# Kernel optimization log

Hardware: AMD Instinct MI355X
Metric: run time of the kernel (lower is better)

## Reference

```python
import jax, jax.numpy as jnp
import numpy as np

ALPHA = 4.0  # spikingjelly surrogate.Sigmoid default

@jax.custom_vjp
def spike(x):
    return (x >= 0.0).astype(x.dtype)

def _spike_fwd(x):
    return spike(x), x

def _spike_bwd(x, g):
    s = jax.nn.sigmoid(ALPHA * x)
    return (g * ALPHA * s * (1.0 - s),)

spike.defvjp(_spike_fwd, _spike_bwd)

def lif(x, v0, v_th=1.0, tau=2.0):
    # Multi-step LIF over leading time axis. v' = v + (x - v)/tau; hard reset to 0; detach_reset.
    def step(v, xt):
        v = v + (xt - v) / tau
        s = spike(v - v_th)
        v = v * (1.0 - jax.lax.stop_gradient(s))
        return v, s
    v_end, s = jax.lax.scan(step, v0, x)
    return s, v_end

def bn_eval(x, gamma, beta, mean, var, eps=1e-5):
    # x: [T,B,C,N], stats over channel dim C (axis 2)
    inv = gamma / jnp.sqrt(var + eps)
    return x * inv.reshape(1, 1, -1, 1) + (beta - mean * inv).reshape(1, 1, -1, 1)

def setup_inputs() -> dict:
    key = jax.random.key(0)
    ks = jax.random.split(key, 24)
    T, B, C, H, W = 4, 16, 512, 16, 16
    d = {}
    d['x'] = jax.random.normal(ks[0], (T, B, C, H, W), dtype=jnp.float32)
    d['res_attn'] = jnp.zeros((1,), dtype=jnp.float32)
    sc = 1.0 / np.sqrt(C)
    for i, p in enumerate(['q', 'k', 'v']):
        d[p + '_w'] = jax.random.normal(ks[1 + i], (C, C), dtype=jnp.float32) * sc
    names = ['q', 'k', 'v', 'p']
    for i, p in enumerate(names):
        d[p + '_gamma'] = jax.random.uniform(ks[4 + i], (C,), minval=0.8, maxval=1.2, dtype=jnp.float32)
        d[p + '_beta'] = jax.random.normal(ks[8 + i], (C,), dtype=jnp.float32) * 0.1
        d[p + '_mean'] = jax.random.normal(ks[12 + i], (C,), dtype=jnp.float32) * 0.1
        d[p + '_var'] = jax.random.uniform(ks[16 + i], (C,), minval=0.5, maxval=1.5, dtype=jnp.float32)
    d['p_w'] = jax.random.normal(ks[20], (C, C), dtype=jnp.float32) * sc
    d['p_b'] = jax.random.normal(ks[21], (C,), dtype=jnp.float32) * 0.02
    return d

def reference(x, res_attn, q_w, q_gamma, q_beta, q_mean, q_var,
              k_w, k_gamma, k_beta, k_mean, k_var,
              v_w, v_gamma, v_beta, v_mean, v_var,
              p_w, p_b, p_gamma, p_beta, p_mean, p_var):
    T, B, C, H, W = x.shape
    N = H * W
    xf = x.reshape(T, B, C, N)
    v0 = jnp.zeros((B, C, N), dtype=x.dtype)

    def qkv_branch(w, g, b, m, va):
        y = jnp.einsum('oc,tbcn->tbon', w, xf)  # 1x1 conv over flattened T*B
        y = bn_eval(y, g, b, m, va)
        s, _ = lif(y, v0)
        return s

    q = qkv_branch(q_w, q_gamma, q_beta, q_mean, q_var)
    k = qkv_branch(k_w, k_gamma, k_beta, k_mean, k_var)
    v = qkv_branch(v_w, v_gamma, v_beta, v_mean, v_var)

    kv = jnp.einsum('tbcn,tbcm->tbnm', k, v)           # k^T @ v : [T,B,N,N]
    a = jnp.einsum('tbcn,tbnm->tbcm', q, kv) * 0.125   # q @ (k^T v), scale
    a, _ = lif(a, v0, v_th=0.5)                        # attn_lif

    y = jnp.einsum('oc,tbcn->tbon', p_w, a) + p_b.reshape(1, 1, -1, 1)
    y = bn_eval(y, p_gamma, p_beta, p_mean, p_var).reshape(T, B, C, H, W)

    v0_sp = jnp.zeros((B, C, H, W), dtype=x.dtype)
    s1, v_end = lif(y, v0_sp)      # first proj_lif call
    s2, _ = lif(s1, v_end)         # second proj_lif call: membrane state persists (stateful node)
    return s2, v
```

## Files before the change

kernel.cpp:

```cpp
#include <hip/hip_runtime.h>
#include <hip/hip_bf16.h>

#define TT 4
#define BB 16
#define CC 512
#define NN 256

typedef short short8 __attribute__((ext_vector_type(8)));
typedef _Float16 h8 __attribute__((ext_vector_type(8)));
typedef float f32x4 __attribute__((ext_vector_type(4)));
typedef float fl4 __attribute__((ext_vector_type(4)));
typedef unsigned short us4 __attribute__((ext_vector_type(4)));

__device__ __forceinline__ unsigned short bf_hi(float x) {
    unsigned u = __float_as_uint(x);
    return (unsigned short)((u + 0x7FFFu + ((u >> 16) & 1u)) >> 16);
}
__device__ __forceinline__ float bf_f(unsigned short h) {
    return __uint_as_float(((unsigned)h) << 16);
}
__device__ __forceinline__ void glds16(const void* g, void* l) {
    __builtin_amdgcn_global_load_lds(
        (const __attribute__((address_space(1))) unsigned int*)g,
        (__attribute__((address_space(3))) unsigned int*)l, 16, 0, 0);
}
__device__ __forceinline__ int csw(int c, int rkey) {
    return (c & ~63) | ((((c >> 3) & 7) ^ (rkey & 7)) << 3) | (c & 7);
}

__global__ __launch_bounds__(256) void prep_k(
    const float* __restrict__ x,
    const float* __restrict__ w0, const float* __restrict__ w1,
    const float* __restrict__ w2, const float* __restrict__ w3,
    unsigned short* __restrict__ xh, unsigned short* __restrict__ xl,
    unsigned short* __restrict__ wsplit)
{
    const int bid = blockIdx.x;
    const int tid = threadIdx.x;
    if (bid < 4096) {
        __shared__ float Tt[64][33];
        const int tb = bid >> 6, rem = bid & 63;
        const int c0 = (rem >> 3) * 64, n0 = (rem & 7) * 32;
        const int t = tb >> 4, b = tb & 15;
        {
            int row = tid >> 2, seg = tid & 3;
            const float* sp = x + ((size_t)tb * CC + c0 + row) * NN + n0 + seg * 8;
            fl4 v0 = *(const fl4*)sp;
            fl4 v1 = *(const fl4*)(sp + 4);
#pragma unroll
            for (int j = 0; j < 4; ++j) {
                Tt[row][seg * 8 + j] = v0[j];
                Tt[row][seg * 8 + 4 + j] = v1[j];
            }
        }
        __syncthreads();
        {
            int n = tid >> 3, co = tid & 7;
            int c = c0 + co * 8;
            short8 hi, lo;
#pragma unroll
            for (int j = 0; j < 8; ++j) {
                float f = Tt[co * 8 + j][n];
                unsigned short h = bf_hi(f);
                hi[j] = (short)h;
                lo[j] = (short)bf_hi(f - bf_f(h));
            }
            int nn = n0 + n;
            int key = (nn & 1) * 4 + t;
            size_t dst = (((size_t)b * NN + nn) * TT + t) * CC
                       + (c & ~63) + (((((c >> 3) & 7) ^ (key & 7))) << 3);
            *(short8*)(xh + dst) = hi;
            *(short8*)(xl + dst) = lo;
        }
    } else {
        const int wb = bid - 4096;
        const int m = wb >> 7;
        const int idx = wb & 127;
        const float* src = (m == 0) ? w0 : (m == 1) ? w1 : (m == 2) ? w2 : w3;
        unsigned short* dh = wsplit + (size_t)m * 2 * CC * CC;
        unsigned short* dl = dh + (size_t)CC * CC;
        const int flat = idx * 2048 + tid * 8;
        const int o = flat >> 9, c = flat & 511;
        const float* sp = src + flat;
        fl4 v0 = *(const fl4*)sp;
        fl4 v1 = *(const fl4*)(sp + 4);
        short8 hi, lo;
#pragma unroll
        for (int j = 0; j < 8; ++j) {
            float f = (j < 4) ? v0[j] : v1[j - 4];
            unsigned short h = bf_hi(f);
            hi[j] = (short)h;
            lo[j] = (short)bf_hi(f - bf_f(h));
        }
        size_t dst = (size_t)o * CC + (c & ~63) + ((((c >> 3) & 7) ^ (o & 7)) << 3);
        *(short8*)(dh + dst) = hi;
        *(short8*)(dl + dst) = lo;
    }
}

__global__ __launch_bounds__(256, 4) void gemm_qkv_f(
    const unsigned short* __restrict__ w8,
    const unsigned short* __restrict__ Bh, const unsigned short* __restrict__ Bl,
    const float* __restrict__ qg, const float* __restrict__ qb,
    const float* __restrict__ qm, const float* __restrict__ qva,
    const float* __restrict__ kg, const float* __restrict__ kbe,
    const float* __restrict__ km, const float* __restrict__ kva,
    const float* __restrict__ vg, const float* __restrict__ vb,
    const float* __restrict__ vm, const float* __restrict__ vva,
    const float* __restrict__ qw, const float* __restrict__ kw,
    const float* __restrict__ vw, const float* __restrict__ xf,
    unsigned short* __restrict__ qo, unsigned short* __restrict__ ktr,
    unsigned short* __restrict__ vtr, float* __restrict__ outv)
{
    const int bid = blockIdx.x;
    const int orig = (bid & 7) * 384 + (bid >> 3);
    const int cb = orig / 12;
    const int ob = orig - cb * 12;
    const int mat = ob >> 2;
    const int o0 = (ob & 3) * 128;
    const int col0 = cb * 64;
    const int b  = cb >> 4;
    const int n0 = (cb & 15) * 16;
    const unsigned short* Ah = w8 + (size_t)mat * 2 * CC * CC;
    const unsigned short* Alg = Ah + (size_t)CC * CC;

    const int tid = threadIdx.x, lane = tid & 63, wid = tid >> 6;
    const int l16 = lane & 15, kb = lane >> 4;
    const int sx = l16 & 7;

    __shared__ __align__(16) char raw[32768];

    const int srow = lane >> 3, sslot = lane & 7;
    const unsigned short* sect =
        (wid == 0) ? Ah + (size_t)o0 * CC :
        (wid == 1) ? Ah + (size_t)(o0 + 64) * CC :
        (wid == 2) ? Bh + (size_t)col0 * CC :
                     Bl + (size_t)col0 * CC;
    const unsigned short* gsrc = sect + (size_t)srow * CC + sslot * 8;
    char* ldsb = raw + wid * 8192;

    f32x4 acc[2][4];
#pragma unroll
    for (int r = 0; r < 2; ++r)
#pragma unroll
        for (int c = 0; c < 4; ++c) acc[r][c] = (f32x4){0.f, 0.f, 0.f, 0.f};

    for (int ks = 0; ks < 8; ++ks) {
        const int k0 = ks * 64;
        short8 alv[2][2];
#pragma unroll
        for (int ksub = 0; ksub < 2; ++ksub)
#pragma unroll
            for (int r = 0; r < 2; ++r)
                alv[ksub][r] = *(const short8*)(Alg
                    + (size_t)(o0 + wid * 32 + r * 16 + l16) * CC
                    + k0 + (((ksub * 4 + kb) ^ sx) << 3));
#pragma unroll
        for (int i = 0; i < 8; ++i)
            glds16(gsrc + (size_t)(i * 8) * CC + k0, ldsb + i * 1024);
        __syncthreads();
#pragma unroll
        for (int ksub = 0; ksub < 2; ++ksub) {
            const int soff = ((ksub * 4 + kb) ^ sx) << 4;
            short8 ah[2], bh[4], bl[4];
#pragma unroll
            for (int r = 0; r < 2; ++r) {
                const int ra = (wid * 32 + r * 16 + l16) * 128 + soff;
                ah[r] = *(const short8*)(raw + ra);
            }
#pragma unroll
            for (int c = 0; c < 4; ++c) {
                const int rb = (c * 16 + l16) * 128 + soff;
                bh[c] = *(const short8*)(raw + 16384 + rb);
                bl[c] = *(const short8*)(raw + 24576 + rb);
            }
#pragma unroll
            for (int r = 0; r < 2; ++r)
#pragma unroll
                for (int c = 0; c < 4; ++c)
                    acc[r][c] = __builtin_amdgcn_mfma_f32_16x16x32_bf16(ah[r], bh[c], acc[r][c], 0, 0, 0);
#pragma unroll
            for (int r = 0; r < 2; ++r)
#pragma unroll
                for (int c = 0; c < 4; ++c)
                    acc[r][c] = __builtin_amdgcn_mfma_f32_16x16x32_bf16(alv[ksub][r], bh[c], acc[r][c], 0, 0, 0);
#pragma unroll
            for (int r = 0; r < 2; ++r)
#pragma unroll
                for (int c = 0; c < 4; ++c)
                    acc[r][c] = __builtin_amdgcn_mfma_f32_16x16x32_bf16(ah[r], bl[c], acc[r][c], 0, 0, 0);
        }
        __syncthreads();
    }

    float* Yf = (float*)raw;
#pragma unroll
    for (int r = 0; r < 2; ++r)
#pragma unroll
        for (int c = 0; c < 4; ++c) {
            const int col = c * 16 + l16;
#pragma unroll
            for (int g = 0; g < 4; ++g) {
                const int row = wid * 32 + r * 16 + kb * 4 + g;
                Yf[row * 64 + (col ^ (((row >> 2) & 7) << 2))] = acc[r][c][g];
            }
        }
    __syncthreads();

    const float* gg = (mat == 0) ? qg : (mat == 1) ? kg : vg;
    const float* be = (mat == 0) ? qb : (mat == 1) ? kbe : vb;
    const float* mu = (mat == 0) ? qm : (mat == 1) ? km : vm;
    const float* va = (mat == 0) ? qva : (mat == 1) ? kva : vva;
    const float* wsel = (mat == 0) ? qw : (mat == 1) ? kw : vw;

    const int lo2  = tid >> 3;
    const int rsel = (tid >> 2) & 1;
    const int ln2  = tid & 3;
    const float M1 = 2e-4f;

    float inv[2], bbv[2];
#pragma unroll
    for (int i = 0; i < 2; ++i) {
        int oo = o0 + lo2 * 4 + rsel * 2 + i;
        double invd = (double)gg[oo] / sqrt((double)va[oo] + 1e-5);
        inv[i] = (float)invd;
        bbv[i] = (float)((double)be[oo] - (double)mu[oo] * invd);
    }

    unsigned long long s1b = 0;
    unsigned fmask = 0;
#pragma unroll
    for (int i = 0; i < 2; ++i) {
        const int row = lo2 * 4 + rsel * 2 + i;
        const int rk = ((row >> 2) & 7) << 2;
#pragma unroll
        for (int j = 0; j < 4; ++j) {
            fl4 yv = *(const fl4*)&Yf[row * 64 + (((ln2 * 4 + j) * 4) ^ rk)];
            float vv = 0.f;
#pragma unroll
            for (int t = 0; t < TT; ++t) {
                float yy = yv[t] * inv[i] + bbv[i];
                vv += (yy - vv) * 0.5f;
                float d = vv - 1.0f;
                if (d < M1 && d > -M1) fmask |= 1u << (i * 4 + j);
                if (d >= 0.0f) { s1b |= 1ull << ((i * 4 + j) * 4 + t); vv = 0.f; }
            }
        }
    }

    unsigned long long ball = __ballot(fmask != 0);
    while (ball) {
        int src = __ffsll(ball) - 1;
        ball &= ball - 1;
        unsigned fm = (unsigned)__shfl((int)fmask, src);
        int slo2 = wid * 8 + (src >> 3);
        int srsel = (src >> 2) & 1, sln = src & 3;
        while (fm) {
            int cell = __ffs(fm) - 1;
            fm &= fm - 1;
            int ci = cell >> 2, cj = cell & 3;
            int oo = o0 + slo2 * 4 + srsel * 2 + ci, nn = n0 + sln * 4 + cj;
            double a0 = 0, a1 = 0, a2 = 0, a3 = 0;
            const float* wrow = wsel + (size_t)oo * CC;
            for (int c = lane; c < CC; c += 64) {
                double wv = (double)wrow[c];
                a0 += wv * (double)xf[(((size_t)(0 * BB + b) * CC + c) * NN) + nn];
                a1 += wv * (double)xf[(((size_t)(1 * BB + b) * CC + c) * NN) + nn];
                a2 += wv * (double)xf[(((size_t)(2 * BB + b) * CC + c) * NN) + nn];
                a3 += wv * (double)xf[(((size_t)(3 * BB + b) * CC + c) * NN) + nn];
            }
#pragma unroll
            for (int off = 32; off > 0; off >>= 1) {
                a0 += __shfl_xor(a0, off);
                a1 += __shfl_xor(a1, off);
                a2 += __shfl_xor(a2, off);
                a3 += __shfl_xor(a3, off);
            }
            if (lane == src) {
                double inv_ = (double)gg[oo] / sqrt((double)va[oo] + 1e-5);
                double bb_  = (double)be[oo] - (double)mu[oo] * inv_;
                s1b &= ~(0xFull << (cell * 4));
                double aa[4] = {a0, a1, a2, a3};
                double vv = 0.0;
#pragma unroll
                for (int t = 0; t < TT; ++t) {
                    double yy = aa[t] * inv_ + bb_;
                    vv += (yy - vv) * 0.5;
                    if (vv >= 1.0) { s1b |= 1ull << (cell * 4 + t); vv = 0.0; }
                }
            }
        }
    }

    if (mat == 0) {
#pragma unroll
        for (int t = 0; t < TT; ++t) {
            const size_t tb = (size_t)(t * BB + b);
#pragma unroll
            for (int i = 0; i < 2; ++i) {
                us4 pk;
#pragma unroll
                for (int j = 0; j < 4; ++j)
                    pk[j] = ((s1b >> ((i * 4 + j) * 4 + t)) & 1ull) ? (unsigned short)0x3C00 : (unsigned short)0;
                *(us4*)(qo + (tb * CC + o0 + lo2 * 4 + rsel * 2 + i) * NN + n0 + ln2 * 4) = pk;
            }
        }
    } else {
        unsigned short* tr = (mat == 1) ? ktr : vtr;
        unsigned short* Tss = (unsigned short*)raw;
        __syncthreads();
#pragma unroll
        for (int t = 0; t < TT; ++t)
#pragma unroll
            for (int j = 0; j < 4; ++j) {
                unsigned p0 = ((s1b >> ((0 * 4 + j) * 4 + t)) & 1ull) ? 0x3F80u : 0u;
                unsigned p1 = ((s1b >> ((1 * 4 + j) * 4 + t)) & 1ull) ? 0x3F80u : 0u;
                *(unsigned*)&Tss[t * 2176 + (ln2 * 4 + j) * 136 + lo2 * 4 + rsel * 2] =
                    p0 | (p1 << 16);
            }
        __syncthreads();
        {
            const int nrow = tid >> 4, seg = tid & 15;
#pragma unroll
            for (int t = 0; t < TT; ++t) {
                const unsigned short* sp = Tss + t * 2176 + nrow * 136 + seg * 8;
                short8 w0 = *(const short8*)sp;
                unsigned short* dst = tr + ((size_t)(t * BB + b) * NN + n0 + nrow) * CC + o0 + seg * 8;
                *(short8*)dst = w0;
            }
        }
        if (mat == 2) {
#pragma unroll
            for (int t = 0; t < TT; ++t) {
                const size_t tb = (size_t)(t * BB + b);
#pragma unroll
                for (int i = 0; i < 2; ++i) {
                    fl4 f;
#pragma unroll
                    for (int j = 0; j < 4; ++j)
                        f[j] = ((s1b >> ((i * 4 + j) * 4 + t)) & 1ull) ? 1.f : 0.f;
                    *(fl4*)(outv + (tb * CC + o0 + lo2 * 4 + rsel * 2 + i) * NN + n0 + ln2 * 4) = f;
                }
            }
        }
    }
}

__global__ __launch_bounds__(256) void gemm_p_f(
    const unsigned short* __restrict__ Ah, const unsigned short* __restrict__ Al,
    const unsigned short* __restrict__ Bhb,
    const float* __restrict__ gg, const float* __restrict__ be,
    const float* __restrict__ mu, const float* __restrict__ va,
    const float* __restrict__ pb, const float* __restrict__ pw,
    const unsigned short* __restrict__ abf, float* __restrict__ out)
{
    const int bid = blockIdx.x;
    const int orig = (bid & 7) * 128 + (bid >> 3);
    const int ob = orig & 3, cb = orig >> 2;
    const int o0 = ob * 128, col0 = cb * 64;
    const int b = cb >> 4, n0 = (cb & 15) * 16;
    const int tid = threadIdx.x, lane = tid & 63, wid = tid >> 6;
    const int l16 = lane & 15, kb = lane >> 4;
    const int sx = l16 & 7;

    __shared__ __align__(16) char raw[32768];

    const int srow = lane >> 3, sslot = lane & 7;
    const unsigned short* gsrc;
    char* ldsb;
    int nglds;
    if (wid == 0)      { gsrc = Ah + (size_t)o0 * CC;        ldsb = raw;         nglds = 8; }
    else if (wid == 1) { gsrc = Ah + (size_t)(o0 + 64) * CC; ldsb = raw + 8192;  nglds = 8; }
    else if (wid == 2) { gsrc = Bhb + (size_t)col0 * CC;     ldsb = raw + 16384; nglds = 4; }
    else               { gsrc = Bhb + (size_t)(col0 + 32) * CC; ldsb = raw + 20480; nglds = 4; }
    gsrc += (size_t)srow * CC + sslot * 8;

    f32x4 acc[2][4];
#pragma unroll
    for (int r = 0; r < 2; ++r)
#pragma unroll
        for (int c = 0; c < 4; ++c) acc[r][c] = (f32x4){0.f, 0.f, 0.f, 0.f};

    for (int ks = 0; ks < 8; ++ks) {
        const int k0 = ks * 64;
        short8 alv[2][2];
#pragma unroll
        for (int ksub = 0; ksub < 2; ++ksub) {
            const int kof = k0 + (((ksub * 4 + kb) ^ sx) << 3);
#pragma unroll
            for (int r = 0; r < 2; ++r)
                alv[ksub][r] = *(const short8*)(Al
                    + (size_t)(o0 + wid * 32 + r * 16 + l16) * CC + kof);
        }
#pragma unroll
        for (int i = 0; i < 8; ++i)
            if (i < nglds)
                glds16(gsrc + (size_t)(i * 8) * CC + k0, ldsb + i * 1024);
        __syncthreads();
#pragma unroll
        for (int ksub = 0; ksub < 2; ++ksub) {
            const int soff = ((ksub * 4 + kb) ^ sx) << 4;
            short8 ah[2], bh[4];
#pragma unroll
            for (int r = 0; r < 2; ++r) {
                const int ra = (wid * 32 + r * 16 + l16) * 128 + soff;
                ah[r] = *(const short8*)(raw + ra);
            }
#pragma unroll
            for (int c = 0; c < 4; ++c) {
                const int rb = (c * 16 + l16) * 128 + soff;
                bh[c] = *(const short8*)(raw + 16384 + rb);
            }
#pragma unroll
            for (int r = 0; r < 2; ++r)
#pragma unroll
                for (int c = 0; c < 4; ++c)
                    acc[r][c] = __builtin_amdgcn_mfma_f32_16x16x32_bf16(ah[r], bh[c], acc[r][c], 0, 0, 0);
#pragma unroll
            for (int r = 0; r < 2; ++r)
#pragma unroll
                for (int c = 0; c < 4; ++c)
                    acc[r][c] = __builtin_amdgcn_mfma_f32_16x16x32_bf16(alv[ksub][r], bh[c], acc[r][c], 0, 0, 0);
        }
        __syncthreads();
    }

    float* Yf = (float*)raw;
#pragma unroll
    for (int r = 0; r < 2; ++r)
#pragma unroll
        for (int c = 0; c < 4; ++c) {
            const int col = c * 16 + l16;
#pragma unroll
            for (int g = 0; g < 4; ++g) {
                const int row = wid * 32 + r * 16 + kb * 4 + g;
                Yf[row * 64 + (col ^ (((row >> 2) & 7) << 2))] = acc[r][c][g];
            }
        }
    __syncthreads();

    const int lo2  = tid >> 3;
    const int rsel = (tid >> 2) & 1;
    const int ln2  = tid & 3;
    const float M1 = 2e-4f;

    float inv[2], bbv[2], pbo[2];
#pragma unroll
    for (int i = 0; i < 2; ++i) {
        int oo = o0 + lo2 * 4 + rsel * 2 + i;
        double invd = (double)gg[oo] / sqrt((double)va[oo] + 1e-5);
        inv[i] = (float)invd;
        bbv[i] = (float)((double)be[oo] - (double)mu[oo] * invd);
        pbo[i] = pb[oo];
    }

    unsigned long long s2b = 0;
    unsigned fmask = 0;
#pragma unroll
    for (int i = 0; i < 2; ++i) {
        const int row = lo2 * 4 + rsel * 2 + i;
        const int rk = ((row >> 2) & 7) << 2;
#pragma unroll
        for (int j = 0; j < 4; ++j) {
            fl4 yv = *(const fl4*)&Yf[row * 64 + (((ln2 * 4 + j) * 4) ^ rk)];
            float vv = 0.f;
            unsigned s1loc = 0;
#pragma unroll
            for (int t = 0; t < TT; ++t) {
                float yy = (yv[t] + pbo[i]) * inv[i] + bbv[i];
                vv += (yy - vv) * 0.5f;
                float d = vv - 1.0f;
                if (d < M1 && d > -M1) fmask |= 1u << (i * 4 + j);
                if (d >= 0.0f) { s1loc |= 1u << t; vv = 0.f; }
            }
            float v2 = vv;
#pragma unroll
            for (int t = 0; t < TT; ++t) {
                float s1 = ((s1loc >> t) & 1u) ? 1.f : 0.f;
                v2 += (s1 - v2) * 0.5f;
                float d = v2 - 1.0f;
                if (d < M1 && d > -M1) fmask |= 1u << (i * 4 + j);
                if (d >= 0.0f) { s2b |= 1ull << ((i * 4 + j) * 4 + t); v2 = 0.f; }
            }
        }
    }

    unsigned long long ball = __ballot(fmask != 0);
    while (ball) {
        int src = __ffsll(ball) - 1;
        ball &= ball - 1;
        unsigned fm = (unsigned)__shfl((int)fmask, src);
        int slo2 = wid * 8 + (src >> 3);
        int srsel = (src >> 2) & 1, sln = src & 3;
        while (fm) {
            int cell = __ffs(fm) - 1;
            fm &= fm - 1;
            int ci = cell >> 2, cj = cell & 3;
            int oo = o0 + slo2 * 4 + srsel * 2 + ci, nn = n0 + sln * 4 + cj;
            double a0 = 0, a1 = 0, a2 = 0, a3 = 0;
            const float* wrow = pw + (size_t)oo * CC;
            const int key0 = (nn & 1) * 4;
            for (int c = lane; c < CC; c += 64) {
                double wv = (double)wrow[c];
                size_t rb = ((size_t)b * NN + nn) * TT;
                if (abf[(rb + 0) * CC + csw(c, key0 + 0)]) a0 += wv;
                if (abf[(rb + 1) * CC + csw(c, key0 + 1)]) a1 += wv;
                if (abf[(rb + 2) * CC + csw(c, key0 + 2)]) a2 += wv;
                if (abf[(rb + 3) * CC + csw(c, key0 + 3)]) a3 += wv;
            }
#pragma unroll
            for (int off = 32; off > 0; off >>= 1) {
                a0 += __shfl_xor(a0, off);
                a1 += __shfl_xor(a1, off);
                a2 += __shfl_xor(a2, off);
                a3 += __shfl_xor(a3, off);
            }
            if (lane == src) {
                double inv_ = (double)gg[oo] / sqrt((double)va[oo] + 1e-5);
                double bb_  = (double)be[oo] - (double)mu[oo] * inv_;
                double pb_  = (double)pb[oo];
                s2b &= ~(0xFull << (cell * 4));
                double aa[4] = {a0, a1, a2, a3};
                double vv = 0.0;
                unsigned s1loc = 0;
#pragma unroll
                for (int t = 0; t < TT; ++t) {
                    double yy = (aa[t] + pb_) * inv_ + bb_;
                    vv += (yy - vv) * 0.5;
                    if (vv >= 1.0) { s1loc |= 1u << t; vv = 0.0; }
                }
                double v2 = vv;
#pragma unroll
                for (int t = 0; t < TT; ++t) {
                    double s1 = ((s1loc >> t) & 1u) ? 1.0 : 0.0;
                    v2 += (s1 - v2) * 0.5;
                    if (v2 >= 1.0) { s2b |= 1ull << (cell * 4 + t); v2 = 0.0; }
                }
            }
        }
    }

#pragma unroll
    for (int t = 0; t < TT; ++t) {
        const size_t tb = (size_t)(t * BB + b);
#pragma unroll
        for (int i = 0; i < 2; ++i) {
            fl4 f;
#pragma unroll
            for (int j = 0; j < 4; ++j)
                f[j] = ((s2b >> ((i * 4 + j) * 4 + t)) & 1ull) ? 1.f : 0.f;
            *(fl4*)(out + (tb * CC + o0 + lo2 * 4 + rsel * 2 + i) * NN + n0 + ln2 * 4) = f;
        }
    }
}

__global__ __launch_bounds__(256) void k2_kv(
    const unsigned short* __restrict__ kt, const unsigned short* __restrict__ vt,
    unsigned short* __restrict__ kvf)
{
    const int bid = blockIdx.x;
    const int rest = bid >> 3;
    const int tb = (bid & 7) + 8 * (rest >> 4);
    const int mn = rest & 15;
    const int m0 = (mn & 3) * 64, n0 = (mn >> 2) * 64;
    const int tid = threadIdx.x, lane = tid & 63, wid = tid >> 6;
    const int wn = wid >> 1, wm = wid & 1;
    const int l16 = lane & 15, kb = lane >> 4;
    __shared__ unsigned short Kt[64][72];
    __shared__ unsigned short Vt[64][72];
    f32x4 acc[2][2];
#pragma unroll
    for (int a = 0; a < 2; ++a)
#pragma unroll
        for (int c = 0; c < 2; ++c) acc[a][c] = (f32x4){0.f, 0.f, 0.f, 0.f};

    for (int ks = 0; ks < 8; ++ks) {
        const int c0 = ks * 64;
#pragma unroll
        for (int i = tid; i < 1024; i += 256) {
            int which = i >> 9, r = (i >> 3) & 63, s = i & 7;
            const unsigned short* sp = (which ? vt : kt) +
                ((size_t)tb * NN + (which ? m0 : n0) + r) * CC + c0 + s * 8;
            unsigned short (*dst)[72] = which ? Vt : Kt;
            *(short8*)(&dst[r][s * 8]) = *(const short8*)sp;
        }
        __syncthreads();
#pragma unroll
        for (int ksub = 0; ksub < 2; ++ksub) {
            const int co = ksub * 32 + kb * 8;
            short8 a0 = *(const short8*)&Kt[wn * 32 + l16][co];
            short8 a1 = *(const short8*)&Kt[wn * 32 + 16 + l16][co];
            short8 b0 = *(const short8*)&Vt[wm * 32 + l16][co];
            short8 b1 = *(const short8*)&Vt[wm * 32 + 16 + l16][co];
            acc[0][0] = __builtin_amdgcn_mfma_f32_16x16x32_bf16(a0, b0, acc[0][0], 0, 0, 0);
            acc[0][1] = __builtin_amdgcn_mfma_f32_16x16x32_bf16(a0, b1, acc[0][1], 0, 0, 0);
            acc[1][0] = __builtin_amdgcn_mfma_f32_16x16x32_bf16(a1, b0, acc[1][0], 0, 0, 0);
            acc[1][1] = __builtin_amdgcn_mfma_f32_16x16x32_bf16(a1, b1, acc[1][1], 0, 0, 0);
        }
        __syncthreads();
    }
#pragma unroll
    for (int fr = 0; fr < 2; ++fr)
#pragma unroll
        for (int fc = 0; fc < 2; ++fc) {
            int n = n0 + wn * 32 + fr * 16 + kb * 4;
            int m = m0 + wm * 32 + fc * 16 + l16;
            us4 pk;
#pragma unroll
            for (int rg = 0; rg < 4; ++rg) {
                union { _Float16 h; unsigned short u; } cv;
                cv.h = (_Float16)acc[fr][fc][rg];
                pk[rg] = cv.u;
            }
            *(us4*)&kvf[((size_t)tb * NN + m) * NN + n] = pk;
        }
}

__global__ __launch_bounds__(256) void k3_attn(
    const unsigned short* __restrict__ qf, const unsigned short* __restrict__ kvf,
    unsigned short* __restrict__ abf)
{
    const int bid = blockIdx.x;
    const int rest = bid >> 3;
    const int b = (bid & 7) + 8 * (rest >> 5);
    const int cm = rest & 31;
    const int c0 = (cm & 7) * 64, m0 = (cm >> 3) * 64;
    const int tid = threadIdx.x, lane = tid & 63, wid = tid >> 6;
    const int wc = wid >> 1, wm = wid & 1;
    const int l16 = lane & 15, kb = lane >> 4;
    __shared__ unsigned short Qt[TT][64][40];
    __shared__ unsigned short Mt[TT][64][40];
    f32x4 acc[TT][2][2];
#pragma unroll
    for (int t = 0; t < TT; ++t)
#pragma unroll
        for (int fr = 0; fr < 2; ++fr)
#pragma unroll
            for (int fc = 0; fc < 2; ++fc) acc[t][fr][fc] = (f32x4){0.f, 0.f, 0.f, 0.f};

    for (int ks = 0; ks < 8; ++ks) {
        const int nk0 = ks * 32;
#pragma unroll
        for (int i = tid; i < 2048; i += 256) {
            int which = i >> 10, rem = i & 1023;
            int t = rem >> 8, r = (rem >> 2) & 63, s = rem & 3;
            if (which == 0) {
                const unsigned short* sp = qf + ((size_t)(t * BB + b) * CC + c0 + r) * NN + nk0 + s * 8;
                *(short8*)(&Qt[t][r][s * 8]) = *(const short8*)sp;
            } else {
                const unsigned short* sp = kvf + ((size_t)(t * BB + b) * NN + m0 + r) * NN + nk0 + s * 8;
                *(short8*)(&Mt[t][r][s * 8]) = *(const short8*)sp;
            }
        }
        __syncthreads();
#pragma unroll
        for (int t = 0; t < TT; ++t) {
            h8 a0 = *(const h8*)&Qt[t][wc * 32 + l16][kb * 8];
            h8 a1 = *(const h8*)&Qt[t][wc * 32 + 16 + l16][kb * 8];
            h8 b0 = *(const h8*)&Mt[t][wm * 32 + l16][kb * 8];
            h8 b1 = *(const h8*)&Mt[t][wm * 32 + 16 + l16][kb * 8];
            acc[t][0][0] = __builtin_amdgcn_mfma_f32_16x16x32_f16(a0, b0, acc[t][0][0], 0, 0, 0);
            acc[t][0][1] = __builtin_amdgcn_mfma_f32_16x16x32_f16(a0, b1, acc[t][0][1], 0, 0, 0);
            acc[t][1][0] = __builtin_amdgcn_mfma_f32_16x16x32_f16(a1, b0, acc[t][1][0], 0, 0, 0);
            acc[t][1][1] = __builtin_amdgcn_mfma_f32_16x16x32_f16(a1, b1, acc[t][1][1], 0, 0, 0);
        }
        __syncthreads();
    }

#pragma unroll
    for (int fr = 0; fr < 2; ++fr)
#pragma unroll
        for (int fc = 0; fc < 2; ++fc) {
            const int m = m0 + wm * 32 + fc * 16 + l16;
            const int cbase = c0 + wc * 32 + fr * 16 + kb * 4;
            const int key0 = (m & 1) * 4;
            us4 pk[TT];
#pragma unroll
            for (int rg = 0; rg < 4; ++rg) {
                float vv = 0.f;
#pragma unroll
                for (int t = 0; t < TT; ++t) {
                    float a = acc[t][fr][fc][rg] * 0.125f;
                    vv += (a - vv) * 0.5f;
                    if (vv >= 0.5f) { pk[t][rg] = 0x3F80; vv = 0.f; }
                    else pk[t][rg] = 0;
                }
            }
#pragma unroll
            for (int t = 0; t < TT; ++t)
                *(us4*)&abf[(((size_t)b * NN + m) * TT + t) * CC + csw(cbase, key0 + t)] = pk[t];
        }
}

extern "C" void kernel_launch(void* const* d_in, const int* in_sizes, int n_in,
                              void* d_out, int out_size, void* d_ws, size_t ws_size,
                              hipStream_t stream)
{
    const float* x    = (const float*)d_in[0];
    const float* q_w  = (const float*)d_in[2];
    const float* k_w  = (const float*)d_in[3];
    const float* v_w  = (const float*)d_in[4];
    const float* q_g  = (const float*)d_in[5];
    const float* q_b  = (const float*)d_in[6];
    const float* q_m  = (const float*)d_in[7];
    const float* q_v  = (const float*)d_in[8];
    const float* k_g  = (const float*)d_in[9];
    const float* k_b  = (const float*)d_in[10];
    const float* k_m  = (const float*)d_in[11];
    const float* k_v  = (const float*)d_in[12];
    const float* v_g  = (const float*)d_in[13];
    const float* v_b  = (const float*)d_in[14];
    const float* v_m  = (const float*)d_in[15];
    const float* v_v  = (const float*)d_in[16];
    const float* p_g  = (const float*)d_in[17];
    const float* p_be = (const float*)d_in[18];
    const float* p_m  = (const float*)d_in[19];
    const float* p_v  = (const float*)d_in[20];
    const float* p_w  = (const float*)d_in[21];
    const float* p_b  = (const float*)d_in[22];

    const size_t ELEMS = (size_t)TT * BB * CC * NN;
    float* out_s2 = (float*)d_out;
    float* out_v  = out_s2 + ELEMS;

    unsigned char* ws8 = (unsigned char*)d_ws;
    unsigned short* xh   = (unsigned short*)ws8;
    unsigned short* xl   = (unsigned short*)(ws8 + 16777216ull);
    unsigned short* w8   = (unsigned short*)(ws8 + 33554432ull);
    unsigned short* qf16 = (unsigned short*)(ws8 + 37748736ull);
    unsigned short* kt   = (unsigned short*)(ws8 + 54525952ull);
    unsigned short* vt   = (unsigned short*)(ws8 + 71303168ull);
    unsigned short* kvf  = (unsigned short*)(ws8 + 88080384ull);
    unsigned short* abf  = (unsigned short*)(ws8 + 104857600ull);

    const size_t WSZ = (size_t)CC * CC;
    unsigned short* wph = w8 + 6 * WSZ;
    unsigned short* wpl = w8 + 7 * WSZ;

    dim3 blk(256);
    prep_k<<<4608, blk, 0, stream>>>(x, q_w, k_w, v_w, p_w, xh, xl, w8);

    gemm_qkv_f<<<3072, blk, 0, stream>>>(w8, xh, xl,
                                         q_g, q_b, q_m, q_v,
                                         k_g, k_b, k_m, k_v,
                                         v_g, v_b, v_m, v_v,
                                         q_w, k_w, v_w, x,
                                         qf16, kt, vt, out_v);

    k2_kv<<<1024, blk, 0, stream>>>(kt, vt, kvf);
    k3_attn<<<512, blk, 0, stream>>>(qf16, kvf, abf);

    gemm_p_f<<<1024, blk, 0, stream>>>(wph, wpl, abf,
                                       p_g, p_be, p_m, p_v, p_b, p_w,
                                       abf, out_s2);
}
```

Measured before the change: 182.4 us.

## Double-buffer B tiles in LDS and load A-high weights directly to registers

The QKV projection GEMM now reads the high-part weight tile straight from global memory into registers, as it already did for the low part. LDS then holds only the Bh/Bl activation tiles, split across four waves. LDS is double-buffered so the next k-step's async global-to-LDS loads are issued before the current MFMAs run, and one barrier per iteration is removed. This hides load latency but adds more global register loads per wave and more register pressure.

```diff
diff --git a/kernel.cpp b/kernel.cpp
--- a/kernel.cpp
+++ b/kernel.cpp
@@ -121,8 +121,8 @@
     const int col0 = cb * 64;
     const int b  = cb >> 4;
     const int n0 = (cb & 15) * 16;
-    const unsigned short* Ah = w8 + (size_t)mat * 2 * CC * CC;
-    const unsigned short* Alg = Ah + (size_t)CC * CC;
+    const unsigned short* Ahg = w8 + (size_t)mat * 2 * CC * CC;
+    const unsigned short* Alg = Ahg + (size_t)CC * CC;
 
     const int tid = threadIdx.x, lane = tid & 63, wid = tid >> 6;
     const int l16 = lane & 15, kb = lane >> 4;
@@ -132,53 +132,60 @@
 
     const int srow = lane >> 3, sslot = lane & 7;
     const unsigned short* sect =
-        (wid == 0) ? Ah + (size_t)o0 * CC :
-        (wid == 1) ? Ah + (size_t)(o0 + 64) * CC :
-        (wid == 2) ? Bh + (size_t)col0 * CC :
-                     Bl + (size_t)col0 * CC;
+        (wid == 0) ? Bh + (size_t)col0 * CC :
+        (wid == 1) ? Bh + (size_t)(col0 + 32) * CC :
+        (wid == 2) ? Bl + (size_t)col0 * CC :
+                     Bl + (size_t)(col0 + 32) * CC;
     const unsigned short* gsrc = sect + (size_t)srow * CC + sslot * 8;
-    char* ldsb = raw + wid * 8192;
+    const int sectoff = wid * 4096;
 
     f32x4 acc[2][4];
 #pragma unroll
     for (int r = 0; r < 2; ++r)
 #pragma unroll
         for (int c = 0; c < 4; ++c) acc[r][c] = (f32x4){0.f, 0.f, 0.f, 0.f};
+
+#pragma unroll
+    for (int i = 0; i < 4; ++i)
+        glds16(gsrc + (size_t)(i * 8) * CC, raw + sectoff + i * 1024);
+    __syncthreads();
 
     for (int ks = 0; ks < 8; ++ks) {
         const int k0 = ks * 64;
-        short8 alv[2][2];
-#pragma unroll
-        for (int ksub = 0; ksub < 2; ++ksub)
-#pragma unroll
-            for (int r = 0; r < 2; ++r)
-                alv[ksub][r] = *(const short8*)(Alg
-                    + (size_t)(o0 + wid * 32 + r * 16 + l16) * CC
-                    + k0 + (((ksub * 4 + kb) ^ sx) << 3));
-#pragma unroll
-        for (int i = 0; i < 8; ++i)
-            glds16(gsrc + (size_t)(i * 8) * CC + k0, ldsb + i * 1024);
-        __syncthreads();
+        char* buf = raw + (ks & 1) * 16384;
+        short8 ahv[2][2], alv[2][2];
+#pragma unroll
+        for (int ksub = 0; ksub < 2; ++ksub) {
+            const int kof = k0 + (((ksub * 4 + kb) ^ sx) << 3);
+#pragma unroll
+            for (int r = 0; r < 2; ++r) {
+                const size_t arow = (size_t)(o0 + wid * 32 + r * 16 + l16) * CC;
+                ahv[ksub][r] = *(const short8*)(Ahg + arow + kof);
+                alv[ksub][r] = *(const short8*)(Alg + arow + kof);
+            }
+        }
+        if (ks < 7) {
+            char* db = raw + ((ks + 1) & 1) * 16384 + sectoff;
+            const unsigned short* gs = gsrc + (ks + 1) * 64;
+#pragma unroll
+            for (int i = 0; i < 4; ++i)
+                glds16(gs + (size_t)(i * 8) * CC, db + i * 1024);
+        }
 #pragma unroll
         for (int ksub = 0; ksub < 2; ++ksub) {
             const int soff = ((ksub * 4 + kb) ^ sx) << 4;
-            short8 ah[2], bh[4], bl[4];
-#pragma unroll
-            for (int r = 0; r < 2; ++r) {
-                const int ra = (wid * 32 + r * 16 + l16) * 128 + soff;
-                ah[r] = *(const short8*)(raw + ra);
-            }
+            short8 bh[4], bl[4];
 #pragma unroll
             for (int c = 0; c < 4; ++c) {
                 const int rb = (c * 16 + l16) * 128 + soff;
-                bh[c] = *(const short8*)(raw + 16384 + rb);
-                bl[c] = *(const short8*)(raw + 24576 + rb);
+                bh[c] = *(const short8*)(buf + rb);
+                bl[c] = *(const short8*)(buf + 8192 + rb);
             }
 #pragma unroll
             for (int r = 0; r < 2; ++r)
 #pragma unroll
                 for (int c = 0; c < 4; ++c)
-                    acc[r][c] = __builtin_amdgcn_mfma_f32_16x16x32_bf16(ah[r], bh[c], acc[r][c], 0, 0, 0);
+                    acc[r][c] = __builtin_amdgcn_mfma_f32_16x16x32_bf16(ahv[ksub][r], bh[c], acc[r][c], 0, 0, 0);
 #pragma unroll
             for (int r = 0; r < 2; ++r)
 #pragma unroll
@@ -188,7 +195,7 @@
             for (int r = 0; r < 2; ++r)
 #pragma unroll
                 for (int c = 0; c < 4; ++c)
-                    acc[r][c] = __builtin_amdgcn_mfma_f32_16x16x32_bf16(ah[r], bl[c], acc[r][c], 0, 0, 0);
+                    acc[r][c] = __builtin_amdgcn_mfma_f32_16x16x32_bf16(ahv[ksub][r], bl[c], acc[r][c], 0, 0, 0);
         }
         __syncthreads();
     }
```

Result: slower. 189.0 us (+3.6%).
